# Performance work log

Hardware: AMD Instinct MI355X
Metric: run time of the kernel (lower is better)

## Reference

```python
import jax, jax.numpy as jnp
import numpy as np

N_NODES = 50000
N_EDGES = 800000
IN_FEATS = 128
HIDDEN = 128
NUM_CLASSES = 47


def setup_inputs() -> dict:
    key = jax.random.key(0)
    k1, k2, k3, k4 = jax.random.split(key, 4)
    features = jax.random.normal(k1, (N_NODES, IN_FEATS), dtype=jnp.float32)
    edge_index = jax.random.randint(k2, (2, N_EDGES), 0, N_NODES, dtype=jnp.int32)
    # Glorot-style init for weights, zeros for bias (DGL GraphConv defaults)
    W1 = jax.random.normal(k3, (IN_FEATS, HIDDEN), dtype=jnp.float32) * (1.0 / np.sqrt(IN_FEATS))
    b1 = jnp.zeros((HIDDEN,), dtype=jnp.float32)
    W2 = jax.random.normal(k4, (HIDDEN, NUM_CLASSES), dtype=jnp.float32) * (1.0 / np.sqrt(HIDDEN))
    b2 = jnp.zeros((NUM_CLASSES,), dtype=jnp.float32)
    return {"features": features, "edge_index": edge_index,
            "W1": W1, "b1": b1, "W2": W2, "b2": b2}


def _graph_conv(x, W, b, src, dst, norm_src, norm_dst, n_nodes):
    # DGL GraphConv, norm='both': D_dst^{-1/2} A D_src^{-1/2} (X W) + b
    h = (x * norm_src[:, None]) @ W            # transform before aggregation
    agg = jax.ops.segment_sum(h[src], dst, num_segments=n_nodes)
    return agg * norm_dst[:, None] + b


def reference(features, edge_index, W1, b1, W2, b2):
    src, dst = edge_index[0], edge_index[1]
    n = features.shape[0]
    ones = jnp.ones((src.shape[0],), dtype=features.dtype)
    deg_out = jax.ops.segment_sum(ones, src, num_segments=n)
    deg_in = jax.ops.segment_sum(ones, dst, num_segments=n)
    norm_src = jax.lax.rsqrt(jnp.clip(deg_out, 1.0))   # d_out^{-1/2}, clamp >= 1
    norm_dst = jax.lax.rsqrt(jnp.clip(deg_in, 1.0))    # d_in^{-1/2}, clamp >= 1

    h = _graph_conv(features, W1, b1, src, dst, norm_src, norm_dst, n)
    h = jax.nn.relu(h)
    out = _graph_conv(h, W2, b2, src, dst, norm_src, norm_dst, n)
    return out
```

## Files before the change

kernel.cpp:

```cpp
#include <hip/hip_runtime.h>
#include <hip/hip_fp16.h>

#define N_NODES 50000
#define N_EDGES 800000
#define IN_F 128
#define HID 128
#define NCLS 47
#define H2S 48
#define NB 128
#define CHUNK 6250
#define PDW 12500
#define G1ROWS 256
#define RSB 98
#define RSC 128


typedef _Float16 f16x8 __attribute__((ext_vector_type(8)));
typedef float f32x4 __attribute__((ext_vector_type(4)));

struct __align__(8)  h2x2 { __half2 a, b; };
struct __align__(16) h2x4 { __half2 a, b, c, d; };

__global__ __launch_bounds__(256) void prep_kernel(const float* __restrict__ W1,
                                                   const float* __restrict__ W2,
                                                   __half* __restrict__ W1Th,
                                                   __half* __restrict__ W1Tl,
                                                   __half* __restrict__ W2Th,
                                                   __half* __restrict__ W2Tl,
                                                   int* __restrict__ sync) {
    const int b = blockIdx.x, t = threadIdx.x;
    if (b < 32) {
        const int i0 = b * 512;
        for (int i2 = i0 + t; i2 < i0 + 512; i2 += 256) {
            int cc = i2 >> 7, k = i2 & 127;
            float w = W1[k * HID + cc];
            __half hv = __float2half_rn(w);
            W1Th[i2] = hv;
            W1Tl[i2] = __float2half_rn(w - __half2float(hv));
        }
    } else if (b < 48) {
        const int i0 = (b - 32) * 512;
        for (int i2 = i0 + t; i2 < i0 + 512; i2 += 256) {
            int cc = i2 >> 7, k = i2 & 127;
            float w = (cc < NCLS) ? W2[k * NCLS + cc] : 0.f;
            __half hv = __float2half_rn(w);
            W2Th[i2] = hv;
            W2Tl[i2] = __float2half_rn(w - __half2float(hv));
        }
    } else {
        if (t < 2) sync[t] = 0;
    }
}

__global__ __launch_bounds__(512) void hist_gemm1_kernel(const int* __restrict__ ei,
        unsigned int* __restrict__ Pdst, unsigned int* __restrict__ Psrc,
        const float* __restrict__ X, const __half* __restrict__ W1Th,
        const __half* __restrict__ W1Tl, __half* __restrict__ H1h) {
    __shared__ unsigned int h[PDW];
    const int t = threadIdx.x;
    if (blockIdx.x < 2 * NB) {
        const bool is_src = blockIdx.x >= NB;
        const int chunk = blockIdx.x & (NB - 1);
        const int* ids = is_src ? ei : ei + N_EDGES;
        uint2* h2 = (uint2*)h;
        for (int j = t; j < PDW / 2; j += 512) h2[j] = make_uint2(0u, 0u);
        __syncthreads();
        const int e0 = chunk * CHUNK;
        const int2* e2p = (const int2*)(ids + e0);
        for (int k = t; k < CHUNK / 2; k += 512) {
            int2 v2 = e2p[k];
            atomicAdd(&h[v2.x >> 2], 1u << ((v2.x & 3) * 8));
            atomicAdd(&h[v2.y >> 2], 1u << ((v2.y & 3) * 8));
        }
        __syncthreads();
        unsigned int* P = (is_src ? Psrc : Pdst) + (size_t)chunk * PDW;
        uint2* P2 = (uint2*)P;
        for (int j = t; j < PDW / 2; j += 512) P2[j] = h2[j];
    } else {
        const int lane = t & 63;
        const int wv = t >> 6;
        const int r16 = lane & 15;
        const int kg = lane >> 4;
        const int row0 = (blockIdx.x - 2 * NB) * G1ROWS + wv * 32;
        f32x4 acc[2][8] = {};
#pragma unroll
        for (int s = 0; s < 4; ++s) {
            const int k0 = 32 * s + 8 * kg;
            f16x8 ah[2], al[2];
#pragma unroll
            for (int rt = 0; rt < 2; ++rt) {
                int row = row0 + rt * 16 + r16;
                int rc = row < N_NODES ? row : N_NODES - 1;
                const float4 x0 = *(const float4*)&X[(size_t)rc * IN_F + k0];
                const float4 x1 = *(const float4*)&X[(size_t)rc * IN_F + k0 + 4];
                const float xv[8] = {x0.x, x0.y, x0.z, x0.w,
                                     x1.x, x1.y, x1.z, x1.w};
#pragma unroll
                for (int j = 0; j < 8; ++j) {
                    _Float16 hv = (_Float16)xv[j];
                    ah[rt][j] = hv;
                    al[rt][j] = (_Float16)(xv[j] - (float)hv);
                }
            }
#pragma unroll
            for (int tt = 0; tt < 8; ++tt) {
                const f16x8 bh = *(const f16x8*)&W1Th[(16 * tt + r16) * IN_F + k0];
                const f16x8 bl = *(const f16x8*)&W1Tl[(16 * tt + r16) * IN_F + k0];
#pragma unroll
                for (int rt = 0; rt < 2; ++rt) {
                    acc[rt][tt] = __builtin_amdgcn_mfma_f32_16x16x32_f16(
                        ah[rt], bh, acc[rt][tt], 0, 0, 0);
                    acc[rt][tt] = __builtin_amdgcn_mfma_f32_16x16x32_f16(
                        al[rt], bh, acc[rt][tt], 0, 0, 0);
                    acc[rt][tt] = __builtin_amdgcn_mfma_f32_16x16x32_f16(
                        ah[rt], bl, acc[rt][tt], 0, 0, 0);
                }
            }
        }
#pragma unroll
        for (int rt = 0; rt < 2; ++rt)
#pragma unroll
            for (int j = 0; j < 4; ++j) {
                const int row = row0 + rt * 16 + 4 * kg + j;
                if (row < N_NODES) {
#pragma unroll
                    for (int tt = 0; tt < 8; ++tt)
                        H1h[(size_t)row * HID + 16 * tt + r16] =
                            __float2half_rn(acc[rt][tt][j]);
                }
            }
    }
}

__global__ __launch_bounds__(256) void reduce_scan_kernel(
        unsigned int* __restrict__ Pdst, const unsigned int* __restrict__ Psrc,
        float* __restrict__ norm_src, float* __restrict__ norm_dst,
        int* __restrict__ offsets, int* __restrict__ chunk_sums,
        int* __restrict__ chunk_base, int* __restrict__ sync) {
    __shared__ int sm[256];
    const int t = threadIdx.x;
    const int b = blockIdx.x;
    const int j = b * RSC + t;
    unsigned int run = 0;
    int n0 = 0, n1 = 0, n2 = 0, n3 = 0, tot = 0;
    if (t < RSC && j < PDW) {
#pragma unroll 8
        for (int c = 0; c < NB; ++c) {
            unsigned int v = Pdst[(size_t)c * PDW + j];
            Pdst[(size_t)c * PDW + j] = run;
            run += v;
        }
        n0 = run & 0xff; n1 = (run >> 8) & 0xff;
        n2 = (run >> 16) & 0xff; n3 = (run >> 24) & 0xff;
        tot = n0 + n1 + n2 + n3;
        *(float4*)&norm_dst[4 * j] = make_float4(
            rsqrtf(fmaxf((float)n0, 1.0f)), rsqrtf(fmaxf((float)n1, 1.0f)),
            rsqrtf(fmaxf((float)n2, 1.0f)), rsqrtf(fmaxf((float)n3, 1.0f)));
        unsigned int rs = 0;
#pragma unroll 8
        for (int c = 0; c < NB; ++c) rs += Psrc[(size_t)c * PDW + j];
        int s0 = rs & 0xff, s1 = (rs >> 8) & 0xff;
        int s2 = (rs >> 16) & 0xff, s3 = (rs >> 24) & 0xff;
        *(float4*)&norm_src[4 * j] = make_float4(
            rsqrtf(fmaxf((float)s0, 1.0f)), rsqrtf(fmaxf((float)s1, 1.0f)),
            rsqrtf(fmaxf((float)s2, 1.0f)), rsqrtf(fmaxf((float)s3, 1.0f)));
    }
    sm[t] = (t < RSC) ? tot : 0;
    __syncthreads();
    for (int off = 32; off > 0; off >>= 1) {
        if ((t & 63) < off) sm[t] += sm[t + off];
        __syncthreads();
    }
    if (t == 0)  atomicExch(&chunk_sums[2 * b], sm[0]);
    if (t == 64) atomicExch(&chunk_sums[2 * b + 1], sm[64]);
    __threadfence();
    __syncthreads();
    if (t == 0) atomicAdd(&sync[0], 1);
    if (b == 0) {
        if (t == 0) {
            while (atomicAdd(&sync[0], 0) < RSB) __builtin_amdgcn_s_sleep(8);
        }
        __syncthreads();
        __threadfence();
        int v = (t < 2 * RSB) ? atomicAdd(&chunk_sums[t], 0) : 0;
        sm[t] = v;
        __syncthreads();
        for (int off = 1; off < 256; off <<= 1) {
            int u = (t >= off) ? sm[t - off] : 0;
            __syncthreads();
            sm[t] += u;
            __syncthreads();
        }
        if (t < 2 * RSB) atomicExch(&chunk_base[t], sm[t] - v);
        __threadfence();
        __syncthreads();
        if (t == 0) {
            offsets[N_NODES] = N_EDGES;
            atomicExch(&sync[1], 1);
        }
    }
    if (t == 0) {
        while (atomicAdd(&sync[1], 0) == 0) __builtin_amdgcn_s_sleep(8);
    }
    __syncthreads();
    __threadfence();
    if (t == 0) sm[0] = atomicAdd(&chunk_base[2 * b], 0);
    __syncthreads();
    const int E = sm[0];
    __syncthreads();
    sm[t] = (t < RSC) ? tot : 0;
    __syncthreads();
    for (int off = 1; off < 256; off <<= 1) {
        int u = (t >= off) ? sm[t - off] : 0;
        __syncthreads();
        sm[t] += u;
        __syncthreads();
    }
    if (t < RSC && j < PDW) {
        const int base0 = E + sm[t] - tot;
        *(int4*)&offsets[4 * j] = make_int4(base0, base0 + n0,
                                            base0 + n0 + n1,
                                            base0 + n0 + n1 + n2);
    }
}

__global__ __launch_bounds__(512) void fill_kernel(const int* __restrict__ src,
        const int* __restrict__ dst, const int* __restrict__ offsets,
        const unsigned int* __restrict__ Pdst, int* __restrict__ csr_src) {
    __shared__ __align__(16) unsigned int cur[PDW];
    const int t = threadIdx.x;
    const int chunk = blockIdx.x;
    uint2* c2 = (uint2*)cur;
    for (int j = t; j < PDW / 2; j += 512) c2[j] = make_uint2(0u, 0u);
    __syncthreads();
    const unsigned int* base = Pdst + (size_t)chunk * PDW;
    const int e0 = chunk * CHUNK;
    const int2* d2p = (const int2*)(dst + e0);
    const int2* s2p = (const int2*)(src + e0);
    for (int k = t; k < CHUNK / 2; k += 512) {
        int2 d2 = d2p[k];
        int2 s2 = s2p[k];
        {
            const int d = d2.x;
            const int sh = (d & 3) * 8;
            const unsigned int bw = base[d >> 2];
            const int off = offsets[d];
            unsigned int old = atomicAdd(&cur[d >> 2], 1u << sh);
            csr_src[off + (int)((bw >> sh) & 0xffu) + (int)((old >> sh) & 0xffu)] = s2.x;
        }
        {
            const int d = d2.y;
            const int sh = (d & 3) * 8;
            const unsigned int bw = base[d >> 2];
            const int off = offsets[d];
            unsigned int old = atomicAdd(&cur[d >> 2], 1u << sh);
            csr_src[off + (int)((bw >> sh) & 0xffu) + (int)((old >> sh) & 0xffu)] = s2.y;
        }
    }
}

__global__ __launch_bounds__(512) void gather1_gemm2_kernel(
        const __half* __restrict__ H1h, const int* __restrict__ offsets,
        const int* __restrict__ csr_src, const float* __restrict__ b1,
        const float* __restrict__ norm_src, const float* __restrict__ norm_dst,
        const __half* __restrict__ W2Th, const __half* __restrict__ W2Tl,
        __half* __restrict__ H2h) {
    __shared__ __align__(16) __half As[16][136];
    const int t = threadIdx.x;
    const int lane = t & 63;
    const int w = t >> 6;
    const int q = lane >> 4;
    const int fl = lane & 15;
    const int row0 = blockIdx.x * 16;
    for (int rr = 0; rr < 2; ++rr) {
        const int lr = 2 * w + rr;
        const int row = row0 + lr;
        const int beg = offsets[row], end = offsets[row + 1];
        float a0 = 0.f, a1 = 0.f, a2 = 0.f, a3 = 0.f;
        float a4 = 0.f, a5 = 0.f, a6 = 0.f, a7 = 0.f;
        for (int base = beg; base < end; base += 64) {
            int idx = 0;
            float nsv = 0.f;
            if (base + lane < end) {
                idx = csr_src[base + lane];
                nsv = norm_src[idx];
            }
            const int cnt = min(end - base, 64);
            for (int j = 0; j < cnt; j += 16) {
                int e0 = j + q, e1 = j + 4 + q, e2 = j + 8 + q, e3 = j + 12 + q;
                int s0 = __shfl(idx, e0);  float n0 = __shfl(nsv, e0);
                int s1 = __shfl(idx, e1);  float n1 = __shfl(nsv, e1);
                int s2 = __shfl(idx, e2);  float n2 = __shfl(nsv, e2);
                int s3 = __shfl(idx, e3);  float n3 = __shfl(nsv, e3);
                h2x4 v0 = *(const h2x4*)&H1h[(size_t)s0 * HID + 8 * fl];
                h2x4 v1 = *(const h2x4*)&H1h[(size_t)s1 * HID + 8 * fl];
                h2x4 v2 = *(const h2x4*)&H1h[(size_t)s2 * HID + 8 * fl];
                h2x4 v3 = *(const h2x4*)&H1h[(size_t)s3 * HID + 8 * fl];
                float2 f;
                f = __half22float2(v0.a); a0 = fmaf(f.x, n0, a0); a1 = fmaf(f.y, n0, a1);
                f = __half22float2(v0.b); a2 = fmaf(f.x, n0, a2); a3 = fmaf(f.y, n0, a3);
                f = __half22float2(v0.c); a4 = fmaf(f.x, n0, a4); a5 = fmaf(f.y, n0, a5);
                f = __half22float2(v0.d); a6 = fmaf(f.x, n0, a6); a7 = fmaf(f.y, n0, a7);
                f = __half22float2(v1.a); a0 = fmaf(f.x, n1, a0); a1 = fmaf(f.y, n1, a1);
                f = __half22float2(v1.b); a2 = fmaf(f.x, n1, a2); a3 = fmaf(f.y, n1, a3);
                f = __half22float2(v1.c); a4 = fmaf(f.x, n1, a4); a5 = fmaf(f.y, n1, a5);
                f = __half22float2(v1.d); a6 = fmaf(f.x, n1, a6); a7 = fmaf(f.y, n1, a7);
                f = __half22float2(v2.a); a0 = fmaf(f.x, n2, a0); a1 = fmaf(f.y, n2, a1);
                f = __half22float2(v2.b); a2 = fmaf(f.x, n2, a2); a3 = fmaf(f.y, n2, a3);
                f = __half22float2(v2.c); a4 = fmaf(f.x, n2, a4); a5 = fmaf(f.y, n2, a5);
                f = __half22float2(v2.d); a6 = fmaf(f.x, n2, a6); a7 = fmaf(f.y, n2, a7);
                f = __half22float2(v3.a); a0 = fmaf(f.x, n3, a0); a1 = fmaf(f.y, n3, a1);
                f = __half22float2(v3.b); a2 = fmaf(f.x, n3, a2); a3 = fmaf(f.y, n3, a3);
                f = __half22float2(v3.c); a4 = fmaf(f.x, n3, a4); a5 = fmaf(f.y, n3, a5);
                f = __half22float2(v3.d); a6 = fmaf(f.x, n3, a6); a7 = fmaf(f.y, n3, a7);
            }
        }
        a0 += __shfl_xor(a0, 16); a1 += __shfl_xor(a1, 16);
        a2 += __shfl_xor(a2, 16); a3 += __shfl_xor(a3, 16);
        a4 += __shfl_xor(a4, 16); a5 += __shfl_xor(a5, 16);
        a6 += __shfl_xor(a6, 16); a7 += __shfl_xor(a7, 16);
        a0 += __shfl_xor(a0, 32); a1 += __shfl_xor(a1, 32);
        a2 += __shfl_xor(a2, 32); a3 += __shfl_xor(a3, 32);
        a4 += __shfl_xor(a4, 32); a5 += __shfl_xor(a5, 32);
        a6 += __shfl_xor(a6, 32); a7 += __shfl_xor(a7, 32);
        if (lane < 16) {
            float nd = norm_dst[row], ns = norm_src[row];
            float4 bA = *(const float4*)&b1[8 * fl];
            float4 bB = *(const float4*)&b1[8 * fl + 4];
            float o0 = fmaxf(fmaf(a0, nd, bA.x), 0.f) * ns;
            float o1 = fmaxf(fmaf(a1, nd, bA.y), 0.f) * ns;
            float o2 = fmaxf(fmaf(a2, nd, bA.z), 0.f) * ns;
            float o3 = fmaxf(fmaf(a3, nd, bA.w), 0.f) * ns;
            float o4 = fmaxf(fmaf(a4, nd, bB.x), 0.f) * ns;
            float o5 = fmaxf(fmaf(a5, nd, bB.y), 0.f) * ns;
            float o6 = fmaxf(fmaf(a6, nd, bB.z), 0.f) * ns;
            float o7 = fmaxf(fmaf(a7, nd, bB.w), 0.f) * ns;
            h2x4 p = {__floats2half2_rn(o0, o1), __floats2half2_rn(o2, o3),
                      __floats2half2_rn(o4, o5), __floats2half2_rn(o6, o7)};
            *(h2x4*)&As[lr][8 * fl] = p;
        }
    }
    __syncthreads();
    if (w < 3) {
        const int r16 = lane & 15;
        const int kg = lane >> 4;
        f32x4 acc = {};
#pragma unroll
        for (int s = 0; s < 4; ++s) {
            const int k0 = 32 * s + 8 * kg;
            const f16x8 a = *(const f16x8*)&As[r16][k0];
            const f16x8 bh = *(const f16x8*)&W2Th[(16 * w + r16) * HID + k0];
            const f16x8 bl = *(const f16x8*)&W2Tl[(16 * w + r16) * HID + k0];
            acc = __builtin_amdgcn_mfma_f32_16x16x32_f16(a, bh, acc, 0, 0, 0);
            acc = __builtin_amdgcn_mfma_f32_16x16x32_f16(a, bl, acc, 0, 0, 0);
        }
#pragma unroll
        for (int jj = 0; jj < 4; ++jj)
            H2h[(size_t)(row0 + 4 * kg + jj) * H2S + 16 * w + r16] =
                __float2half_rn(acc[jj]);
    }
}

__global__ __launch_bounds__(256) void gather2_kernel(const __half* __restrict__ H2h,
        const int* __restrict__ offsets, const int* __restrict__ csr_src,
        const float* __restrict__ b2, const float* __restrict__ norm_dst,
        float* __restrict__ out) {
    const int lane = threadIdx.x & 63;
    const int row = blockIdx.x * 4 + (threadIdx.x >> 6);
    const int beg = offsets[row], end = offsets[row + 1];
    const int cl = min(lane, H2S - 1);
    float acc = 0.f;
    for (int base = beg; base < end; base += 64) {
        int idx = 0;
        float wv = 0.f;
        if (base + lane < end) {
            idx = csr_src[base + lane];
            wv = 1.f;
        }
        const int cnt = min(end - base, 64);
        for (int j = 0; j < cnt; j += 4) {
            int s0 = __shfl(idx, j);     float w0 = __shfl(wv, j);
            int s1 = __shfl(idx, j + 1); float w1 = __shfl(wv, j + 1);
            int s2 = __shfl(idx, j + 2); float w2 = __shfl(wv, j + 2);
            int s3 = __shfl(idx, j + 3); float w3 = __shfl(wv, j + 3);
            float f0 = __half2float(H2h[(size_t)s0 * H2S + cl]);
            float f1 = __half2float(H2h[(size_t)s1 * H2S + cl]);
            float f2 = __half2float(H2h[(size_t)s2 * H2S + cl]);
            float f3 = __half2float(H2h[(size_t)s3 * H2S + cl]);
            acc = fmaf(f0, w0, acc);
            acc = fmaf(f1, w1, acc);
            acc = fmaf(f2, w2, acc);
            acc = fmaf(f3, w3, acc);
        }
    }
    if (lane < NCLS) out[(size_t)row * NCLS + lane] = acc * norm_dst[row] + b2[lane];
}

extern "C" void kernel_launch(void* const* d_in, const int* in_sizes, int n_in,
                              void* d_out, int out_size, void* d_ws, size_t ws_size,
                              hipStream_t stream) {
    const float* X  = (const float*)d_in[0];
    const int*   ei = (const int*)d_in[1];
    const float* W1 = (const float*)d_in[2];
    const float* b1 = (const float*)d_in[3];
    const float* W2 = (const float*)d_in[4];
    const float* b2 = (const float*)d_in[5];
    float* out = (float*)d_out;

    const int* src = ei;
    const int* dst = ei + N_EDGES;

    char* w = (char*)d_ws;
    auto alloc = [&](size_t bytes) {
        char* p = w;
        w += (bytes + 255) & ~(size_t)255;
        return p;
    };
    float*  norm_src   = (float*)alloc(N_NODES * 4);
    float*  norm_dst   = (float*)alloc(N_NODES * 4);
    int*    offsets    = (int*)alloc((N_NODES + 1) * 4);
    int*    csr_src    = (int*)alloc((size_t)N_EDGES * 4);
    int*    chunk_sums = (int*)alloc(2 * RSB * 4);
    int*    chunk_base = (int*)alloc(2 * RSB * 4);
    int*    syncw      = (int*)alloc(2 * 4);
    __half* W1Th       = (__half*)alloc((size_t)IN_F * HID * 2);
    __half* W1Tl       = (__half*)alloc((size_t)IN_F * HID * 2);
    __half* W2Th       = (__half*)alloc((size_t)64 * HID * 2);
    __half* W2Tl       = (__half*)alloc((size_t)64 * HID * 2);
    __half* H1h        = (__half*)alloc((size_t)N_NODES * HID * 2);
    __half* H2h        = (__half*)alloc((size_t)N_NODES * H2S * 2);
    unsigned int* Pdst = (unsigned int*)alloc((size_t)NB * PDW * 4);
    unsigned int* Psrc = (unsigned int*)alloc((size_t)NB * PDW * 4);

    const int g1_blocks = (N_NODES + G1ROWS - 1) / G1ROWS;
    prep_kernel<<<49, 256, 0, stream>>>(W1, W2, W1Th, W1Tl, W2Th, W2Tl, syncw);
    hist_gemm1_kernel<<<2 * NB + g1_blocks, 512, 0, stream>>>(ei, Pdst, Psrc,
                                                              X, W1Th, W1Tl, H1h);
    reduce_scan_kernel<<<RSB, 256, 0, stream>>>(Pdst, Psrc, norm_src, norm_dst,
                                                offsets, chunk_sums, chunk_base,
                                                syncw);
    fill_kernel<<<NB, 512, 0, stream>>>(src, dst, offsets, Pdst, csr_src);
    gather1_gemm2_kernel<<<N_NODES / 16, 512, 0, stream>>>(H1h, offsets, csr_src,
                                                           b1, norm_src, norm_dst,
                                                           W2Th, W2Tl, H2h);
    gather2_kernel<<<N_NODES / 4, 256, 0, stream>>>(H2h, offsets, csr_src, b2,
                                                    norm_dst, out);
}
```

Before: 221.5 us.

## Split fused gather1+GEMM2 into separate kernels and shrink GEMM1 tiles

```diff
diff --git a/kernel.cpp b/kernel.cpp
--- a/kernel.cpp
+++ b/kernel.cpp
@@ -7,10 +7,13 @@
 #define HID 128
 #define NCLS 47
 #define H2S 48
+#define W2C 64
 #define NB 128
 #define CHUNK 6250
 #define PDW 12500
-#define G1ROWS 256
+#define G1ROWS 128
+#define G1B 391
+#define G2ROWS 128
 #define RSB 98
 #define RSC 128
 
@@ -81,54 +84,49 @@
         const int wv = t >> 6;
         const int r16 = lane & 15;
         const int kg = lane >> 4;
-        const int row0 = (blockIdx.x - 2 * NB) * G1ROWS + wv * 32;
-        f32x4 acc[2][8] = {};
+        const int row0 = (blockIdx.x - 2 * NB) * G1ROWS + wv * 16;
+        const int ar = row0 + r16;
+        const int arc = ar < N_NODES ? ar : N_NODES - 1;
+        const float* xp = &X[(size_t)arc * IN_F + 8 * kg];
+        float4 xr[8];
+#pragma unroll
+        for (int s = 0; s < 4; ++s) {
+            xr[2 * s]     = *(const float4*)(xp + 32 * s);
+            xr[2 * s + 1] = *(const float4*)(xp + 32 * s + 4);
+        }
+        f32x4 acc[8] = {};
 #pragma unroll
         for (int s = 0; s < 4; ++s) {
             const int k0 = 32 * s + 8 * kg;
-            f16x8 ah[2], al[2];
-#pragma unroll
-            for (int rt = 0; rt < 2; ++rt) {
-                int row = row0 + rt * 16 + r16;
-                int rc = row < N_NODES ? row : N_NODES - 1;
-                const float4 x0 = *(const float4*)&X[(size_t)rc * IN_F + k0];
-                const float4 x1 = *(const float4*)&X[(size_t)rc * IN_F + k0 + 4];
-                const float xv[8] = {x0.x, x0.y, x0.z, x0.w,
-                                     x1.x, x1.y, x1.z, x1.w};
-#pragma unroll
-                for (int j = 0; j < 8; ++j) {
-                    _Float16 hv = (_Float16)xv[j];
-                    ah[rt][j] = hv;
-                    al[rt][j] = (_Float16)(xv[j] - (float)hv);
-                }
+            const float xv[8] = {xr[2 * s].x, xr[2 * s].y, xr[2 * s].z, xr[2 * s].w,
+                                 xr[2 * s + 1].x, xr[2 * s + 1].y,
+                                 xr[2 * s + 1].z, xr[2 * s + 1].w};
+            f16x8 ah, al;
+#pragma unroll
+            for (int j = 0; j < 8; ++j) {
+                _Float16 hv = (_Float16)xv[j];
+                ah[j] = hv;
+                al[j] = (_Float16)(xv[j] - (float)hv);
             }
 #pragma unroll
             for (int tt = 0; tt < 8; ++tt) {
                 const f16x8 bh = *(const f16x8*)&W1Th[(16 * tt + r16) * IN_F + k0];
                 const f16x8 bl = *(const f16x8*)&W1Tl[(16 * tt + r16) * IN_F + k0];
-#pragma unroll
-                for (int rt = 0; rt < 2; ++rt) {
-                    acc[rt][tt] = __builtin_amdgcn_mfma_f32_16x16x32_f16(
-                        ah[rt], bh, acc[rt][tt], 0, 0, 0);
-                    acc[rt][tt] = __builtin_amdgcn_mfma_f32_16x16x32_f16(
-                        al[rt], bh, acc[rt][tt], 0, 0, 0);
-                    acc[rt][tt] = __builtin_amdgcn_mfma_f32_16x16x32_f16(
-                        ah[rt], bl, acc[rt][tt], 0, 0, 0);
-                }
+                acc[tt] = __builtin_amdgcn_mfma_f32_16x16x32_f16(ah, bh, acc[tt], 0, 0, 0);
+                acc[tt] = __builtin_amdgcn_mfma_f32_16x16x32_f16(al, bh, acc[tt], 0, 0, 0);
+                acc[tt] = __builtin_amdgcn_mfma_f32_16x16x32_f16(ah, bl, acc[tt], 0, 0, 0);
             }
         }
 #pragma unroll
-        for (int rt = 0; rt < 2; ++rt)
-#pragma unroll
-            for (int j = 0; j < 4; ++j) {
-                const int row = row0 + rt * 16 + 4 * kg + j;
-                if (row < N_NODES) {
-#pragma unroll
-                    for (int tt = 0; tt < 8; ++tt)
-                        H1h[(size_t)row * HID + 16 * tt + r16] =
-                            __float2half_rn(acc[rt][tt][j]);
-                }
+        for (int j = 0; j < 4; ++j) {
+            const int row = row0 + 4 * kg + j;
+            if (row < N_NODES) {
+#pragma unroll
+                for (int tt = 0; tt < 8; ++tt)
+                    H1h[(size_t)row * HID + 16 * tt + r16] =
+                        __float2half_rn(acc[tt][j]);
             }
+        }
     }
 }
 
@@ -259,106 +257,125 @@
     }
 }
 
-__global__ __launch_bounds__(512) void gather1_gemm2_kernel(
-        const __half* __restrict__ H1h, const int* __restrict__ offsets,
-        const int* __restrict__ csr_src, const float* __restrict__ b1,
-        const float* __restrict__ norm_src, const float* __restrict__ norm_dst,
-        const __half* __restrict__ W2Th, const __half* __restrict__ W2Tl,
-        __half* __restrict__ H2h) {
-    __shared__ __align__(16) __half As[16][136];
-    const int t = threadIdx.x;
-    const int lane = t & 63;
-    const int w = t >> 6;
+__global__ __launch_bounds__(256) void gather1_kernel(const __half* __restrict__ H1h,
+        const int* __restrict__ offsets, const int* __restrict__ csr_src,
+        const float* __restrict__ b1, const float* __restrict__ norm_src,
+        const float* __restrict__ norm_dst, __half* __restrict__ Hrelu16) {
+    const int lane = threadIdx.x & 63;
     const int q = lane >> 4;
     const int fl = lane & 15;
-    const int row0 = blockIdx.x * 16;
-    for (int rr = 0; rr < 2; ++rr) {
-        const int lr = 2 * w + rr;
-        const int row = row0 + lr;
-        const int beg = offsets[row], end = offsets[row + 1];
-        float a0 = 0.f, a1 = 0.f, a2 = 0.f, a3 = 0.f;
-        float a4 = 0.f, a5 = 0.f, a6 = 0.f, a7 = 0.f;
-        for (int base = beg; base < end; base += 64) {
-            int idx = 0;
-            float nsv = 0.f;
-            if (base + lane < end) {
-                idx = csr_src[base + lane];
-                nsv = norm_src[idx];
+    const int row = blockIdx.x * 4 + (threadIdx.x >> 6);
+    const int beg = offsets[row], end = offsets[row + 1];
+    float a0 = 0.f, a1 = 0.f, a2 = 0.f, a3 = 0.f;
+    float a4 = 0.f, a5 = 0.f, a6 = 0.f, a7 = 0.f;
+    for (int base = beg; base < end; base += 64) {
+        int idx = 0;
+        float nsv = 0.f;
+        if (base + lane < end) {
+            idx = csr_src[base + lane];
+            nsv = norm_src[idx];
+        }
+        const int cnt = min(end - base, 64);
+        for (int j = 0; j < cnt; j += 16) {
+            int e0 = j + q, e1 = j + 4 + q, e2 = j + 8 + q, e3 = j + 12 + q;
+            int s0 = __shfl(idx, e0);  float n0 = __shfl(nsv, e0);
+            int s1 = __shfl(idx, e1);  float n1 = __shfl(nsv, e1);
+            int s2 = __shfl(idx, e2);  float n2 = __shfl(nsv, e2);
+            int s3 = __shfl(idx, e3);  float n3 = __shfl(nsv, e3);
+            h2x4 v0 = *(const h2x4*)&H1h[(size_t)s0 * HID + 8 * fl];
+            h2x4 v1 = *(const h2x4*)&H1h[(size_t)s1 * HID + 8 * fl];
+            h2x4 v2 = *(const h2x4*)&H1h[(size_t)s2 * HID + 8 * fl];
+            h2x4 v3 = *(const h2x4*)&H1h[(size_t)s3 * HID + 8 * fl];
+            float2 f;
+            f = __half22float2(v0.a); a0 = fmaf(f.x, n0, a0); a1 = fmaf(f.y, n0, a1);
+            f = __half22float2(v0.b); a2 = fmaf(f.x, n0, a2); a3 = fmaf(f.y, n0, a3);
+            f = __half22float2(v0.c); a4 = fmaf(f.x, n0, a4); a5 = fmaf(f.y, n0, a5);
+            f = __half22float2(v0.d); a6 = fmaf(f.x, n0, a6); a7 = fmaf(f.y, n0, a7);
+            f = __half22float2(v1.a); a0 = fmaf(f.x, n1, a0); a1 = fmaf(f.y, n1, a1);
+            f = __half22float2(v1.b); a2 = fmaf(f.x, n1, a2); a3 = fmaf(f.y, n1, a3);
+            f = __half22float2(v1.c); a4 = fmaf(f.x, n1, a4); a5 = fmaf(f.y, n1, a5);
+            f = __half22float2(v1.d); a6 = fmaf(f.x, n1, a6); a7 = fmaf(f.y, n1, a7);
+            f = __half22float2(v2.a); a0 = fmaf(f.x, n2, a0); a1 = fmaf(f.y, n2, a1);
+            f = __half22float2(v2.b); a2 = fmaf(f.x, n2, a2); a3 = fmaf(f.y, n2, a3);
+            f = __half22float2(v2.c); a4 = fmaf(f.x, n2, a4); a5 = fmaf(f.y, n2, a5);
+            f = __half22float2(v2.d); a6 = fmaf(f.x, n2, a6); a7 = fmaf(f.y, n2, a7);
+            f = __half22float2(v3.a); a0 = fmaf(f.x, n3, a0); a1 = fmaf(f.y, n3, a1);
+            f = __half22float2(v3.b); a2 = fmaf(f.x, n3, a2); a3 = fmaf(f.y, n3, a3);
+            f = __half22float2(v3.c); a4 = fmaf(f.x, n3, a4); a5 = fmaf(f.y, n3, a5);
+            f = __half22float2(v3.d); a6 = fmaf(f.x, n3, a6); a7 = fmaf(f.y, n3, a7);
+        }
+    }
+    a0 += __shfl_xor(a0, 16); a1 += __shfl_xor(a1, 16);
+    a2 += __shfl_xor(a2, 16); a3 += __shfl_xor(a3, 16);
+    a4 += __shfl_xor(a4, 16); a5 += __shfl_xor(a5, 16);
+    a6 += __shfl_xor(a6, 16); a7 += __shfl_xor(a7, 16);
+    a0 += __shfl_xor(a0, 32); a1 += __shfl_xor(a1, 32);
+    a2 += __shfl_xor(a2, 32); a3 += __shfl_xor(a3, 32);
+    a4 += __shfl_xor(a4, 32); a5 += __shfl_xor(a5, 32);
+    a6 += __shfl_xor(a6, 32); a7 += __shfl_xor(a7, 32);
+    if (lane < 16) {
+        float nd = norm_dst[row], ns = norm_src[row];
+        float4 bA = *(const float4*)&b1[8 * fl];
+        float4 bB = *(const float4*)&b1[8 * fl + 4];
+        float o0 = fmaxf(fmaf(a0, nd, bA.x), 0.f) * ns;
+        float o1 = fmaxf(fmaf(a1, nd, bA.y), 0.f) * ns;
+        float o2 = fmaxf(fmaf(a2, nd, bA.z), 0.f) * ns;
+        float o3 = fmaxf(fmaf(a3, nd, bA.w), 0.f) * ns;
+        float o4 = fmaxf(fmaf(a4, nd, bB.x), 0.f) * ns;
+        float o5 = fmaxf(fmaf(a5, nd, bB.y), 0.f) * ns;
+        float o6 = fmaxf(fmaf(a6, nd, bB.z), 0.f) * ns;
+        float o7 = fmaxf(fmaf(a7, nd, bB.w), 0.f) * ns;
+        h2x4 p = {__floats2half2_rn(o0, o1), __floats2half2_rn(o2, o3),
+                  __floats2half2_rn(o4, o5), __floats2half2_rn(o6, o7)};
+        *(h2x4*)&Hrelu16[(size_t)row * HID + 8 * fl] = p;
+    }
+}
+
+__global__ __launch_bounds__(256) void gemm2_kernel(const __half* __restrict__ Hrelu16,
+                                                    const __half* __restrict__ W2Th,
+                                                    const __half* __restrict__ W2Tl,
+                                                    __half* __restrict__ H2h) {
+    const int lane = threadIdx.x & 63;
+    const int wv = threadIdx.x >> 6;
+    const int r16 = lane & 15;
+    const int kg = lane >> 4;
+    const int row0 = blockIdx.x * G2ROWS + wv * 32;
+    f32x4 acc[2][3] = {};
+#pragma unroll
+    for (int s = 0; s < 4; ++s) {
+        const int k0 = 32 * s + 8 * kg;
+        f16x8 a[2];
+#pragma unroll
+        for (int rt = 0; rt < 2; ++rt) {
+            int row = row0 + rt * 16 + r16;
+            int rc = row < N_NODES ? row : N_NODES - 1;
+            a[rt] = *(const f16x8*)&Hrelu16[(size_t)rc * HID + k0];
+        }
+#pragma unroll
+        for (int tt = 0; tt < 3; ++tt) {
+            const f16x8 bh = *(const f16x8*)&W2Th[(16 * tt + r16) * HID + k0];
+            const f16x8 bl = *(const f16x8*)&W2Tl[(16 * tt + r16) * HID + k0];
+#pragma unroll
+            for (int rt = 0; rt < 2; ++rt) {
+                acc[rt][tt] = __builtin_amdgcn_mfma_f32_16x16x32_f16(
+                    a[rt], bh, acc[rt][tt], 0, 0, 0);
+                acc[rt][tt] = __builtin_amdgcn_mfma_f32_16x16x32_f16(
+                    a[rt], bl, acc[rt][tt], 0, 0, 0);
             }
-            const int cnt = min(end - base, 64);
-            for (int j = 0; j < cnt; j += 16) {
-                int e0 = j + q, e1 = j + 4 + q, e2 = j + 8 + q, e3 = j + 12 + q;
-                int s0 = __shfl(idx, e0);  float n0 = __shfl(nsv, e0);
-                int s1 = __shfl(idx, e1);  float n1 = __shfl(nsv, e1);
-                int s2 = __shfl(idx, e2);  float n2 = __shfl(nsv, e2);
-                int s3 = __shfl(idx, e3);  float n3 = __shfl(nsv, e3);
-                h2x4 v0 = *(const h2x4*)&H1h[(size_t)s0 * HID + 8 * fl];
-                h2x4 v1 = *(const h2x4*)&H1h[(size_t)s1 * HID + 8 * fl];
-                h2x4 v2 = *(const h2x4*)&H1h[(size_t)s2 * HID + 8 * fl];
-                h2x4 v3 = *(const h2x4*)&H1h[(size_t)s3 * HID + 8 * fl];
-                float2 f;
-                f = __half22float2(v0.a); a0 = fmaf(f.x, n0, a0); a1 = fmaf(f.y, n0, a1);
-                f = __half22float2(v0.b); a2 = fmaf(f.x, n0, a2); a3 = fmaf(f.y, n0, a3);
-                f = __half22float2(v0.c); a4 = fmaf(f.x, n0, a4); a5 = fmaf(f.y, n0, a5);
-                f = __half22float2(v0.d); a6 = fmaf(f.x, n0, a6); a7 = fmaf(f.y, n0, a7);
-                f = __half22float2(v1.a); a0 = fmaf(f.x, n1, a0); a1 = fmaf(f.y, n1, a1);
-                f = __half22float2(v1.b); a2 = fmaf(f.x, n1, a2); a3 = fmaf(f.y, n1, a3);
-                f = __half22float2(v1.c); a4 = fmaf(f.x, n1, a4); a5 = fmaf(f.y, n1, a5);
-                f = __half22float2(v1.d); a6 = fmaf(f.x, n1, a6); a7 = fmaf(f.y, n1, a7);
-                f = __half22float2(v2.a); a0 = fmaf(f.x, n2, a0); a1 = fmaf(f.y, n2, a1);
-                f = __half22float2(v2.b); a2 = fmaf(f.x, n2, a2); a3 = fmaf(f.y, n2, a3);
-                f = __half22float2(v2.c); a4 = fmaf(f.x, n2, a4); a5 = fmaf(f.y, n2, a5);
-                f = __half22float2(v2.d); a6 = fmaf(f.x, n2, a6); a7 = fmaf(f.y, n2, a7);
-                f = __half22float2(v3.a); a0 = fmaf(f.x, n3, a0); a1 = fmaf(f.y, n3, a1);
-                f = __half22float2(v3.b); a2 = fmaf(f.x, n3, a2); a3 = fmaf(f.y, n3, a3);
-                f = __half22float2(v3.c); a4 = fmaf(f.x, n3, a4); a5 = fmaf(f.y, n3, a5);
-                f = __half22float2(v3.d); a6 = fmaf(f.x, n3, a6); a7 = fmaf(f.y, n3, a7);
+        }
+    }
+#pragma unroll
+    for (int rt = 0; rt < 2; ++rt)
+#pragma unroll
+        for (int j = 0; j < 4; ++j) {
+            const int row = row0 + rt * 16 + 4 * kg + j;
+            if (row < N_NODES) {
+#pragma unroll
+                for (int tt = 0; tt < 3; ++tt)
+                    H2h[(size_t)row * H2S + 16 * tt + r16] =
+                        __float2half_rn(acc[rt][tt][j]);
             }
         }
-        a0 += __shfl_xor(a0, 16); a1 += __shfl_xor(a1, 16);
-        a2 += __shfl_xor(a2, 16); a3 += __shfl_xor(a3, 16);
-        a4 += __shfl_xor(a4, 16); a5 += __shfl_xor(a5, 16);
-        a6 += __shfl_xor(a6, 16); a7 += __shfl_xor(a7, 16);
-        a0 += __shfl_xor(a0, 32); a1 += __shfl_xor(a1, 32);
-        a2 += __shfl_xor(a2, 32); a3 += __shfl_xor(a3, 32);
-        a4 += __shfl_xor(a4, 32); a5 += __shfl_xor(a5, 32);
-        a6 += __shfl_xor(a6, 32); a7 += __shfl_xor(a7, 32);
-        if (lane < 16) {
-            float nd = norm_dst[row], ns = norm_src[row];
-            float4 bA = *(const float4*)&b1[8 * fl];
-            float4 bB = *(const float4*)&b1[8 * fl + 4];
-            float o0 = fmaxf(fmaf(a0, nd, bA.x), 0.f) * ns;
-            float o1 = fmaxf(fmaf(a1, nd, bA.y), 0.f) * ns;
-            float o2 = fmaxf(fmaf(a2, nd, bA.z), 0.f) * ns;
-            float o3 = fmaxf(fmaf(a3, nd, bA.w), 0.f) * ns;
-            float o4 = fmaxf(fmaf(a4, nd, bB.x), 0.f) * ns;
-            float o5 = fmaxf(fmaf(a5, nd, bB.y), 0.f) * ns;
-            float o6 = fmaxf(fmaf(a6, nd, bB.z), 0.f) * ns;
-            float o7 = fmaxf(fmaf(a7, nd, bB.w), 0.f) * ns;
-            h2x4 p = {__floats2half2_rn(o0, o1), __floats2half2_rn(o2, o3),
-                      __floats2half2_rn(o4, o5), __floats2half2_rn(o6, o7)};
-            *(h2x4*)&As[lr][8 * fl] = p;
-        }
-    }
-    __syncthreads();
-    if (w < 3) {
-        const int r16 = lane & 15;
-        const int kg = lane >> 4;
-        f32x4 acc = {};
-#pragma unroll
-        for (int s = 0; s < 4; ++s) {
-            const int k0 = 32 * s + 8 * kg;
-            const f16x8 a = *(const f16x8*)&As[r16][k0];
-            const f16x8 bh = *(const f16x8*)&W2Th[(16 * w + r16) * HID + k0];
-            const f16x8 bl = *(const f16x8*)&W2Tl[(16 * w + r16) * HID + k0];
-            acc = __builtin_amdgcn_mfma_f32_16x16x32_f16(a, bh, acc, 0, 0, 0);
-            acc = __builtin_amdgcn_mfma_f32_16x16x32_f16(a, bl, acc, 0, 0, 0);
-        }
-#pragma unroll
-        for (int jj = 0; jj < 4; ++jj)
-            H2h[(size_t)(row0 + 4 * kg + jj) * H2S + 16 * w + r16] =
-                __float2half_rn(acc[jj]);
-    }
 }
 
 __global__ __launch_bounds__(256) void gather2_kernel(const __half* __restrict__ H2h,
@@ -425,24 +442,25 @@
     int*    syncw      = (int*)alloc(2 * 4);
     __half* W1Th       = (__half*)alloc((size_t)IN_F * HID * 2);
     __half* W1Tl       = (__half*)alloc((size_t)IN_F * HID * 2);
-    __half* W2Th       = (__half*)alloc((size_t)64 * HID * 2);
-    __half* W2Tl       = (__half*)alloc((size_t)64 * HID * 2);
+    __half* W2Th       = (__half*)alloc((size_t)W2C * HID * 2);
+    __half* W2Tl       = (__half*)alloc((size_t)W2C * HID * 2);
     __half* H1h        = (__half*)alloc((size_t)N_NODES * HID * 2);
+    __half* Hrelu16    = (__half*)alloc((size_t)N_NODES * HID * 2);
     __half* H2h        = (__half*)alloc((size_t)N_NODES * H2S * 2);
     unsigned int* Pdst = (unsigned int*)alloc((size_t)NB * PDW * 4);
     unsigned int* Psrc = (unsigned int*)alloc((size_t)NB * PDW * 4);
 
-    const int g1_blocks = (N_NODES + G1ROWS - 1) / G1ROWS;
+    const int g2_blocks = (N_NODES + G2ROWS - 1) / G2ROWS;
     prep_kernel<<<49, 256, 0, stream>>>(W1, W2, W1Th, W1Tl, W2Th, W2Tl, syncw);
-    hist_gemm1_kernel<<<2 * NB + g1_blocks, 512, 0, stream>>>(ei, Pdst, Psrc,
-                                                              X, W1Th, W1Tl, H1h);
+    hist_gemm1_kernel<<<2 * NB + G1B, 512, 0, stream>>>(ei, Pdst, Psrc,
+                                                        X, W1Th, W1Tl, H1h);
     reduce_scan_kernel<<<RSB, 256, 0, stream>>>(Pdst, Psrc, norm_src, norm_dst,
                                                 offsets, chunk_sums, chunk_base,
                                                 syncw);
     fill_kernel<<<NB, 512, 0, stream>>>(src, dst, offsets, Pdst, csr_src);
-    gather1_gemm2_kernel<<<N_NODES / 16, 512, 0, stream>>>(H1h, offsets, csr_src,
-                                                           b1, norm_src, norm_dst,
-                                                           W2Th, W2Tl, H2h);
+    gather1_kernel<<<N_NODES / 4, 256, 0, stream>>>(H1h, offsets, csr_src, b1,
+                                                    norm_src, norm_dst, Hrelu16);
+    gemm2_kernel<<<g2_blocks, 256, 0, stream>>>(Hrelu16, W2Th, W2Tl, H2h);
     gather2_kernel<<<N_NODES / 4, 256, 0, stream>>>(H2h, offsets, csr_src, b2,
                                                     norm_dst, out);
 }
```

Measured after the change: 229.5 us. 1.04x slower.
